# Kernel tuning notes

Measured on AMD Instinct MI355X. Metric: run time of the kernel, lower is better.

Reference implementation:

```python
import jax, jax.numpy as jnp
import numpy as np

D_MODEL = 1024
NUM_HEADS = 16
D_HEAD = D_MODEL // NUM_HEADS
D_FF = 4096
BATCH = 2
SEQ = 2048
EPS = 1e-5


def setup_inputs() -> dict:
    key = jax.random.key(0)
    ks = jax.random.split(key, 10)
    def tn(k, shape, std):
        # truncated normal in [-3*std, 3*std]
        return std * jax.random.truncated_normal(k, -3.0, 3.0, shape, dtype=jnp.float32)
    sd_attn = float(np.sqrt(2.0 / (D_MODEL + D_MODEL)))
    sd_ff1 = float(np.sqrt(2.0 / (D_MODEL + D_FF)))
    sd_ff2 = float(np.sqrt(2.0 / (D_FF + D_MODEL)))
    return {
        "x": jax.random.normal(ks[0], (BATCH, SEQ, D_MODEL), dtype=jnp.float32),
        "Wq": tn(ks[1], (D_MODEL, D_MODEL), sd_attn),
        "Wk": tn(ks[2], (D_MODEL, D_MODEL), sd_attn),
        "Wv": tn(ks[3], (D_MODEL, D_MODEL), sd_attn),
        "Wo": tn(ks[4], (D_MODEL, D_MODEL), sd_attn),
        "W1": tn(ks[5], (D_FF, D_MODEL), sd_ff1),
        "W2": tn(ks[6], (D_MODEL, D_FF), sd_ff2),
        "W3": tn(ks[7], (D_FF, D_MODEL), sd_ff1),
        "g1": tn(ks[8], (D_MODEL,), 1.0),
        "g2": tn(ks[9], (D_MODEL,), 1.0),
    }


def rmsnorm(x, g):
    xf = x.astype(jnp.float32)
    rms = jnp.sqrt(jnp.mean(xf * xf, axis=-1, keepdims=True) + EPS)
    return (xf / rms * g).astype(x.dtype)


def attention(x, Wq, Wk, Wv, Wo):
    B, S, D = x.shape
    def heads(t):  # [B,S,D] -> [B,H,S,dh]
        return t.reshape(B, S, NUM_HEADS, D_HEAD).transpose(0, 2, 1, 3)
    q = heads(jnp.einsum('oi,bsi->bso', Wq, x))
    k = heads(jnp.einsum('oi,bsi->bso', Wk, x))
    v = heads(jnp.einsum('oi,bsi->bso', Wv, x))
    logits = jnp.einsum('bhqd,bhkd->bhqk', q, k)
    mask = jnp.tril(jnp.ones((S, S), dtype=bool))
    logits = jnp.where(mask, logits, -jnp.inf)
    attn = jax.nn.softmax(logits / jnp.sqrt(jnp.float32(D_HEAD)), axis=-1)
    o = jnp.einsum('bhqk,bhkd->bhqd', attn, v)
    o = o.transpose(0, 2, 1, 3).reshape(B, S, D)
    return jnp.einsum('oi,bsi->bso', Wo, o)


def swiglu(x, W1, W2, W3):
    h1 = jnp.einsum('fi,bsi->bsf', W1, x)
    h3 = jnp.einsum('fi,bsi->bsf', W3, x)
    h = h1 * jax.nn.sigmoid(h1) * h3
    return jnp.einsum('of,bsf->bso', W2, h)


def reference(x, Wq, Wk, Wv, Wo, W1, W2, W3, g1, g2):
    x = x + attention(rmsnorm(x, g1), Wq, Wk, Wv, Wo)
    x = x + swiglu(rmsnorm(x, g2), W1, W2, W3)
    return x
```

## Files before the change

### kernel.cpp

```cpp
#include <hip/hip_runtime.h>
#include <hip/hip_bf16.h>

#define DM 1024
#define NH 16
#define DH 64
#define DFF 4096
#define NBATCH 2
#define SEQL 2048
#define MTOK (NBATCH*SEQL)

typedef float f32x4 __attribute__((ext_vector_type(4)));
typedef __bf16 bf16x8 __attribute__((ext_vector_type(8)));
typedef unsigned short u16;
typedef unsigned int u32;
typedef unsigned short u16x4 __attribute__((ext_vector_type(4)));
typedef unsigned short u16x8 __attribute__((ext_vector_type(8)));
typedef unsigned int u32x4 __attribute__((ext_vector_type(4)));

__device__ __forceinline__ u16 f2bf(float f) {
    u32 u = __builtin_bit_cast(u32, f);
    return (u16)((u + 0x7fffu + ((u >> 16) & 1u)) >> 16);
}
__device__ __forceinline__ float bf2f(u16 h) {
    return __builtin_bit_cast(float, (u32)h << 16);
}
__device__ __forceinline__ f32x4 mfma16(bf16x8 a, bf16x8 b, f32x4 c) {
    return __builtin_amdgcn_mfma_f32_16x16x32_bf16(a, b, c, 0, 0, 0);
}
__device__ __forceinline__ void gload16(const void* g, void* l) {
    __builtin_amdgcn_global_load_lds(
        (const __attribute__((address_space(1))) unsigned int*)g,
        (__attribute__((address_space(3))) unsigned int*)l, 16, 0, 0);
}

template<bool PRE>
__device__ __forceinline__ void gemm_core(
    const u16* __restrict__ Ah, const u16* __restrict__ Al,
    const u16* __restrict__ Bh, const u16* __restrict__ Bl,
    const float* __restrict__ W,
    int K, int m0, int n0,
    u16* lsAh, u16* lsAl, u16* lsBh, u16* lsBl,
    f32x4 acc[4][4])
{
    const int t = threadIdx.x;
    const int lane = t & 63;
    const int wv = t >> 6;
    const int wm = ((t >> 7) & 1) * 64;
    const int wn = ((t >> 6) & 1) * 64;
    const int lrow = lane & 15;
    const int lk = lane >> 4;
    const f32x4 FZ = {0.f, 0.f, 0.f, 0.f};
#pragma unroll
    for (int i = 0; i < 4; ++i)
#pragma unroll
        for (int j = 0; j < 4; ++j) acc[i][j] = FZ;

    for (int k0 = 0; k0 < K; k0 += 64) {
        if (PRE) {
#pragma unroll
            for (int p = 0; p < 4; ++p) {
                const int seg = wv * 4 + p;
                const int row = seg * 8 + (lane >> 3);
                const int g = (lane & 7) ^ (row & 7);
                const size_t sa = (size_t)(m0 + row) * K + k0 + g * 8;
                const size_t sb = (size_t)(n0 + row) * K + k0 + g * 8;
                gload16(Ah + sa, lsAh + seg * 512);
                gload16(Al + sa, lsAl + seg * 512);
                gload16(Bh + sb, lsBh + seg * 512);
                gload16(Bl + sb, lsBl + seg * 512);
            }
        } else {
#pragma unroll
            for (int j = 0; j < 4; ++j) {
                const int row = (t >> 3) + j * 32;
                const int chk = t & 7;
                const size_t src = (size_t)(m0 + row) * K + k0 + chk * 8;
                const int di = row * 64 + ((chk ^ (row & 7)) << 3);
                *reinterpret_cast<u16x8*>(&lsAh[di]) = *reinterpret_cast<const u16x8*>(&Ah[src]);
                *reinterpret_cast<u16x8*>(&lsAl[di]) = *reinterpret_cast<const u16x8*>(&Al[src]);
            }
#pragma unroll
            for (int j = 0; j < 8; ++j) {
                const int id = t + j * 256;
                const int row = id >> 4;
                const int f4 = id & 15;
                const f32x4 wv4 = *reinterpret_cast<const f32x4*>(&W[(size_t)(n0 + row) * K + k0 + f4 * 4]);
                u16x4 hh, ll;
#pragma unroll
                for (int e = 0; e < 4; ++e) {
                    const u16 hi = f2bf(wv4[e]);
                    hh[e] = hi;
                    ll[e] = f2bf(wv4[e] - bf2f(hi));
                }
                const int kc = f4 * 4;
                const int di = row * 64 + ((((kc >> 3) ^ (row & 7))) << 3) + (kc & 7);
                *reinterpret_cast<u16x4*>(&lsBh[di]) = hh;
                *reinterpret_cast<u16x4*>(&lsBl[di]) = ll;
            }
        }
        __syncthreads();
#pragma unroll
        for (int ks = 0; ks < 2; ++ks) {
            bf16x8 ah[4], al[4], bh[4], bl[4];
#pragma unroll
            for (int i = 0; i < 4; ++i) {
                const int ra = wm + i * 16 + lrow;
                const int ia = ra * 64 + ((((lk + ks * 4) ^ (ra & 7))) << 3);
                ah[i] = *reinterpret_cast<const bf16x8*>(&lsAh[ia]);
                al[i] = *reinterpret_cast<const bf16x8*>(&lsAl[ia]);
                const int rb = wn + i * 16 + lrow;
                const int ib = rb * 64 + ((((lk + ks * 4) ^ (rb & 7))) << 3);
                bh[i] = *reinterpret_cast<const bf16x8*>(&lsBh[ib]);
                bl[i] = *reinterpret_cast<const bf16x8*>(&lsBl[ib]);
            }
#pragma unroll
            for (int i = 0; i < 4; ++i)
#pragma unroll
                for (int j = 0; j < 4; ++j) {
                    acc[i][j] = mfma16(ah[i], bh[j], acc[i][j]);
                    acc[i][j] = mfma16(al[i], bh[j], acc[i][j]);
                    acc[i][j] = mfma16(ah[i], bl[j], acc[i][j]);
                }
        }
        __syncthreads();
    }
}

template <class F>
__device__ __forceinline__ void epilogue(const f32x4 acc[4][4], int m0, int n0, F f) {
    const int lane = threadIdx.x & 63;
    const int wm = ((threadIdx.x >> 7) & 1) * 64;
    const int wn = ((threadIdx.x >> 6) & 1) * 64;
#pragma unroll
    for (int i = 0; i < 4; ++i)
#pragma unroll
        for (int j = 0; j < 4; ++j)
#pragma unroll
            for (int r = 0; r < 4; ++r) {
                const int m = m0 + wm + i * 16 + ((lane >> 4) << 2) + r;
                const int o = n0 + wn + j * 16 + (lane & 15);
                f(m, o, acc[i][j][r]);
            }
}

__global__ __launch_bounds__(256) void k_splitw(
    const float* __restrict__ src, u16* __restrict__ dh, u16* __restrict__ dl, int n)
{
    const int i = (blockIdx.x * 256 + threadIdx.x) * 8;
    if (i + 8 > n) return;
    const f32x4 a = *reinterpret_cast<const f32x4*>(src + i);
    const f32x4 b = *reinterpret_cast<const f32x4*>(src + i + 4);
    u16x8 hh, ll;
#pragma unroll
    for (int e = 0; e < 4; ++e) {
        const u16 h0 = f2bf(a[e]);
        hh[e] = h0; ll[e] = f2bf(a[e] - bf2f(h0));
        const u16 h1 = f2bf(b[e]);
        hh[4 + e] = h1; ll[4 + e] = f2bf(b[e] - bf2f(h1));
    }
    *reinterpret_cast<u16x8*>(dh + i) = hh;
    *reinterpret_cast<u16x8*>(dl + i) = ll;
}

__global__ __launch_bounds__(256) void k_rmsnorm(
    const float* __restrict__ x, const float* __restrict__ g,
    u16* __restrict__ oh, u16* __restrict__ ol)
{
    const int row = blockIdx.x * 4 + (threadIdx.x >> 6);
    const int lane = threadIdx.x & 63;
    const float* xr = x + (size_t)row * DM;
    f32x4 v[4];
    float ss = 0.f;
#pragma unroll
    for (int j = 0; j < 4; ++j) {
        v[j] = *reinterpret_cast<const f32x4*>(&xr[(lane + j * 64) * 4]);
        ss += v[j][0] * v[j][0] + v[j][1] * v[j][1] + v[j][2] * v[j][2] + v[j][3] * v[j][3];
    }
#pragma unroll
    for (int off = 32; off > 0; off >>= 1) ss += __shfl_xor(ss, off, 64);
    const float sc = 1.0f / sqrtf(ss * (1.0f / (float)DM) + 1e-5f);
#pragma unroll
    for (int j = 0; j < 4; ++j) {
        const int c0 = (lane + j * 64) * 4;
        const f32x4 gv = *reinterpret_cast<const f32x4*>(&g[c0]);
        u16x4 hh, ll;
#pragma unroll
        for (int e = 0; e < 4; ++e) {
            const float y = v[j][e] * sc * gv[e];
            const u16 hi = f2bf(y);
            hh[e] = hi;
            ll[e] = f2bf(y - bf2f(hi));
        }
        *reinterpret_cast<u16x4*>(&oh[(size_t)row * DM + c0]) = hh;
        *reinterpret_cast<u16x4*>(&ol[(size_t)row * DM + c0]) = ll;
    }
}

template<bool PRE>
__global__ __launch_bounds__(256) void k_qkv(
    const u16* __restrict__ Ah, const u16* __restrict__ Al,
    const float* __restrict__ Wq, const float* __restrict__ Wk, const float* __restrict__ Wv,
    const u16* __restrict__ swqh, const u16* __restrict__ swql,
    const u16* __restrict__ swkh, const u16* __restrict__ swkl,
    const u16* __restrict__ swvh, const u16* __restrict__ swvl,
    u16* __restrict__ qh, u16* __restrict__ ql, u16* __restrict__ kh, u16* __restrict__ kl,
    u16* __restrict__ vth, u16* __restrict__ vtl)
{
    __shared__ __align__(16) u16 lsAh[128 * 64], lsAl[128 * 64], lsBh[128 * 64], lsBl[128 * 64];
    const int m0 = blockIdx.x * 128;
    const int ng = blockIdx.y * 128;
    const int proj = ng >> 10;
    const int n0 = ng & 1023;
    const float* W = (proj == 0) ? Wq : ((proj == 1) ? Wk : Wv);
    const u16* Bh = (proj == 0) ? swqh : ((proj == 1) ? swkh : swvh);
    const u16* Bl = (proj == 0) ? swql : ((proj == 1) ? swkl : swvl);
    f32x4 acc[4][4];
    gemm_core<PRE>(Ah, Al, Bh, Bl, W, DM, m0, n0, lsAh, lsAl, lsBh, lsBl, acc);
    if (proj < 2) {
        u16* oph = (proj == 0) ? qh : kh;
        u16* opl = (proj == 0) ? ql : kl;
        epilogue(acc, m0, n0, [&](int m, int o, float val) {
            const int b = m >> 11, s = m & (SEQL - 1);
            const int hd = o >> 6, d = o & 63;
            const size_t idx = (((size_t)b * NH + hd) * SEQL + s) * DH + d;
            const u16 hi = f2bf(val);
            oph[idx] = hi;
            opl[idx] = f2bf(val - bf2f(hi));
        });
    } else {
        epilogue(acc, m0, n0, [&](int m, int o, float val) {
            const int b = m >> 11, s = m & (SEQL - 1);
            const int hd = o >> 6, d = o & 63;
            const size_t idx = (((size_t)b * NH + hd) * DH + d) * SEQL + s;
            const u16 hi = f2bf(val);
            vth[idx] = hi;
            vtl[idx] = f2bf(val - bf2f(hi));
        });
    }
}

template<bool PRE>
__global__ __launch_bounds__(256) void k_oproj(
    const u16* __restrict__ Ah, const u16* __restrict__ Al,
    const float* __restrict__ Wo, const u16* __restrict__ Bh, const u16* __restrict__ Bl,
    const float* __restrict__ xres, float* __restrict__ out)
{
    __shared__ __align__(16) u16 lsAh[128 * 64], lsAl[128 * 64], lsBh[128 * 64], lsBl[128 * 64];
    const int m0 = blockIdx.x * 128;
    const int n0 = blockIdx.y * 128;
    f32x4 acc[4][4];
    gemm_core<PRE>(Ah, Al, Bh, Bl, Wo, DM, m0, n0, lsAh, lsAl, lsBh, lsBl, acc);
    epilogue(acc, m0, n0, [&](int m, int o, float val) {
        const size_t idx = (size_t)m * DM + o;
        out[idx] = xres[idx] + val;
    });
}

template<bool PRE>
__global__ __launch_bounds__(256) void k_ffn1(
    const u16* __restrict__ Ah, const u16* __restrict__ Al,
    const float* __restrict__ W1, const u16* __restrict__ Bh, const u16* __restrict__ Bl,
    u16* __restrict__ hh, u16* __restrict__ hl)
{
    __shared__ __align__(16) u16 lsAh[128 * 64], lsAl[128 * 64], lsBh[128 * 64], lsBl[128 * 64];
    const int m0 = blockIdx.x * 128;
    const int n0 = blockIdx.y * 128;
    f32x4 acc[4][4];
    gemm_core<PRE>(Ah, Al, Bh, Bl, W1, DM, m0, n0, lsAh, lsAl, lsBh, lsBl, acc);
    epilogue(acc, m0, n0, [&](int m, int o, float val) {
        const size_t idx = (size_t)m * DFF + o;
        const u16 hi = f2bf(val);
        hh[idx] = hi;
        hl[idx] = f2bf(val - bf2f(hi));
    });
}

template<bool PRE>
__global__ __launch_bounds__(256) void k_ffn3(
    const u16* __restrict__ Ah, const u16* __restrict__ Al,
    const float* __restrict__ W3, const u16* __restrict__ Bh, const u16* __restrict__ Bl,
    u16* __restrict__ hh, u16* __restrict__ hl)
{
    __shared__ __align__(16) u16 lsAh[128 * 64], lsAl[128 * 64], lsBh[128 * 64], lsBl[128 * 64];
    const int m0 = blockIdx.x * 128;
    const int n0 = blockIdx.y * 128;
    f32x4 acc[4][4];
    gemm_core<PRE>(Ah, Al, Bh, Bl, W3, DM, m0, n0, lsAh, lsAl, lsBh, lsBl, acc);
    epilogue(acc, m0, n0, [&](int m, int o, float val) {
        const size_t idx = (size_t)m * DFF + o;
        const float h1 = bf2f(hh[idx]) + bf2f(hl[idx]);
        const float sg = 1.0f / (1.0f + expf(-h1));
        const float hv = h1 * sg * val;
        const u16 hi = f2bf(hv);
        hh[idx] = hi;
        hl[idx] = f2bf(hv - bf2f(hi));
    });
}

template<bool PRE>
__global__ __launch_bounds__(256) void k_ffn2(
    const u16* __restrict__ Ah, const u16* __restrict__ Al,
    const float* __restrict__ W2, const u16* __restrict__ Bh, const u16* __restrict__ Bl,
    float* __restrict__ out)
{
    __shared__ __align__(16) u16 lsAh[128 * 64], lsAl[128 * 64], lsBh[128 * 64], lsBl[128 * 64];
    const int m0 = blockIdx.x * 128;
    const int n0 = blockIdx.y * 128;
    f32x4 acc[4][4];
    gemm_core<PRE>(Ah, Al, Bh, Bl, W2, DFF, m0, n0, lsAh, lsAl, lsBh, lsBl, acc);
    epilogue(acc, m0, n0, [&](int m, int o, float val) {
        const size_t idx = (size_t)m * DM + o;
        out[idx] = out[idx] + val;
    });
}

__global__ __launch_bounds__(256) void k_attn(
    const u16* __restrict__ gqh, const u16* __restrict__ gql,
    const u16* __restrict__ gkh, const u16* __restrict__ gkl,
    const u16* __restrict__ gvth, const u16* __restrict__ gvtl,
    u16* __restrict__ aoh, u16* __restrict__ aol)
{
    __shared__ __align__(16) u16 sKh[2][4096], sKl[2][4096], sVh[2][4096], sVl[2][4096];
    __shared__ __align__(16) u32 Pw[4][16 * 64];
    const int t = threadIdx.x, lane = t & 63, wid = t >> 6;
    const int lrow = lane & 15, lk = lane >> 4;
    const int bh = blockIdx.y;
    const int pr = blockIdx.x;
    const size_t base = (size_t)bh * SEQL * DH;
    const f32x4 FZ = {0.f, 0.f, 0.f, 0.f};
    const int b = bh >> 4, hd = bh & 15;

    auto stage = [&](int buf, int kvt) {
        const int kv0 = kvt << 6;
#pragma unroll
        for (int p = 0; p < 2; ++p) {
            const int seg = wid * 2 + p;
            const int row = seg * 8 + (lane >> 3);
            const int g = (lane & 7) ^ (row & 7);
            const size_t sk = base + (size_t)(kv0 + row) * DH + g * 8;
            const size_t sv = base + (size_t)row * SEQL + kv0 + g * 8;
            gload16(gkh + sk, &sKh[buf][seg * 512]);
            gload16(gkl + sk, &sKl[buf][seg * 512]);
            gload16(gvth + sv, &sVh[buf][seg * 512]);
            gload16(gvtl + sv, &sVl[buf][seg * 512]);
        }
    };

    for (int hf = 0; hf < 2; ++hf) {
        const int qt = hf ? (31 - pr) : pr;
        const int qw = qt * 64 + wid * 16;
        bf16x8 Qh[2], Ql[2];
#pragma unroll
        for (int ks = 0; ks < 2; ++ks) {
            const size_t off = base + (size_t)(qw + lrow) * DH + ks * 32 + lk * 8;
            Qh[ks] = *reinterpret_cast<const bf16x8*>(&gqh[off]);
            Ql[ks] = *reinterpret_cast<const bf16x8*>(&gql[off]);
        }
        float mr[4], lr[4];
        f32x4 Oa[4];
#pragma unroll
        for (int r = 0; r < 4; ++r) { mr[r] = -1.0e30f; lr[r] = 0.f; }
#pragma unroll
        for (int n = 0; n < 4; ++n) Oa[n] = FZ;

        const int ntile = qt + 1;
        stage(0, 0);
        __syncthreads();
        int buf = 0;
        for (int kvt = 0; kvt < ntile; ++kvt) {
            if (kvt + 1 < ntile) stage(buf ^ 1, kvt + 1);
            const int kv0 = kvt << 6;
            f32x4 S[4];
#pragma unroll
            for (int nf = 0; nf < 4; ++nf) S[nf] = FZ;
#pragma unroll
            for (int ks = 0; ks < 2; ++ks) {
                bf16x8 kbh[4], kbl[4];
#pragma unroll
                for (int nf = 0; nf < 4; ++nf) {
                    const int row = nf * 16 + lrow;
                    const int idx = row * 64 + (((lk + ks * 4) ^ (row & 7)) << 3);
                    kbh[nf] = *reinterpret_cast<const bf16x8*>(&sKh[buf][idx]);
                    kbl[nf] = *reinterpret_cast<const bf16x8*>(&sKl[buf][idx]);
                }
#pragma unroll
                for (int nf = 0; nf < 4; ++nf) {
                    S[nf] = mfma16(Qh[ks], kbh[nf], S[nf]);
                    S[nf] = mfma16(Ql[ks], kbh[nf], S[nf]);
                    S[nf] = mfma16(Qh[ks], kbl[nf], S[nf]);
                }
            }
#pragma unroll
            for (int r = 0; r < 4; ++r) {
                const int qrow = qw + (lk << 2) + r;
                float rmx = -3.0e38f;
#pragma unroll
                for (int nf = 0; nf < 4; ++nf) {
                    const int col = kv0 + nf * 16 + lrow;
                    const float tv = (col <= qrow) ? S[nf][r] * 0.125f : -3.0e38f;
                    S[nf][r] = tv;
                    rmx = fmaxf(rmx, tv);
                }
#pragma unroll
                for (int off = 8; off > 0; off >>= 1) rmx = fmaxf(rmx, __shfl_xor(rmx, off, 16));
                const float mnew = fmaxf(mr[r], rmx);
                const float alpha = exp2f((mr[r] - mnew) * 1.44269504f);
                mr[r] = mnew;
                float rsum = 0.f;
#pragma unroll
                for (int nf = 0; nf < 4; ++nf) {
                    const float p = exp2f((S[nf][r] - mnew) * 1.44269504f);
                    S[nf][r] = p;
                    rsum += p;
                }
#pragma unroll
                for (int off = 8; off > 0; off >>= 1) rsum += __shfl_xor(rsum, off, 16);
                lr[r] = lr[r] * alpha + rsum;
#pragma unroll
                for (int n = 0; n < 4; ++n) Oa[n][r] *= alpha;
                const int prow = (lk << 2) + r;
#pragma unroll
                for (int nf = 0; nf < 4; ++nf) {
                    const float p = S[nf][r];
                    const u16 phi = f2bf(p);
                    const u16 plo = f2bf(p - bf2f(phi));
                    const int pcol = nf * 16 + lrow;
                    Pw[wid][prow * 64 + ((((pcol >> 3) ^ (prow & 7))) << 3) + (pcol & 7)] =
                        (u32)phi | ((u32)plo << 16);
                }
            }
            asm volatile("s_waitcnt lgkmcnt(0)" ::: "memory");
#pragma unroll
            for (int ks = 0; ks < 2; ++ks) {
                const int row = lrow;
                const int c = (lk + ks * 4) ^ (row & 7);
                const u32* pp = &Pw[wid][row * 64 + (c << 3)];
                const u32x4 w0 = *reinterpret_cast<const u32x4*>(pp);
                const u32x4 w1 = *reinterpret_cast<const u32x4*>(pp + 4);
                union { u16 s[8]; bf16x8 v; } uh, ul;
#pragma unroll
                for (int e = 0; e < 4; ++e) {
                    uh.s[e] = (u16)(w0[e] & 0xffffu); ul.s[e] = (u16)(w0[e] >> 16);
                    uh.s[e + 4] = (u16)(w1[e] & 0xffffu); ul.s[e + 4] = (u16)(w1[e] >> 16);
                }
                bf16x8 vbh[4], vbl[4];
#pragma unroll
                for (int n = 0; n < 4; ++n) {
                    const int vr = n * 16 + lrow;
                    const int idx = vr * 64 + (((lk + ks * 4) ^ (vr & 7)) << 3);
                    vbh[n] = *reinterpret_cast<const bf16x8*>(&sVh[buf][idx]);
                    vbl[n] = *reinterpret_cast<const bf16x8*>(&sVl[buf][idx]);
                }
#pragma unroll
                for (int n = 0; n < 4; ++n) {
                    Oa[n] = mfma16(uh.v, vbh[n], Oa[n]);
                    Oa[n] = mfma16(ul.v, vbh[n], Oa[n]);
                    Oa[n] = mfma16(uh.v, vbl[n], Oa[n]);
                }
            }
            __syncthreads();
            buf ^= 1;
        }
#pragma unroll
        for (int r = 0; r < 4; ++r) {
            const float inv = 1.0f / lr[r];
            const int s = qw + (lk << 2) + r;
#pragma unroll
            for (int n = 0; n < 4; ++n) {
                const float o = Oa[n][r] * inv;
                const int d = hd * 64 + n * 16 + lrow;
                const size_t idx = ((size_t)b * SEQL + s) * DM + d;
                const u16 hi = f2bf(o);
                aoh[idx] = hi;
                aol[idx] = f2bf(o - bf2f(hi));
            }
        }
    }
}

extern "C" void kernel_launch(void* const* d_in, const int* in_sizes, int n_in,
                              void* d_out, int out_size, void* d_ws, size_t ws_size,
                              hipStream_t stream) {
    (void)in_sizes; (void)n_in; (void)out_size;
    const float* x  = (const float*)d_in[0];
    const float* Wq = (const float*)d_in[1];
    const float* Wk = (const float*)d_in[2];
    const float* Wv = (const float*)d_in[3];
    const float* Wo = (const float*)d_in[4];
    const float* W1 = (const float*)d_in[5];
    const float* W2 = (const float*)d_in[6];
    const float* W3 = (const float*)d_in[7];
    const float* g1 = (const float*)d_in[8];
    const float* g2 = (const float*)d_in[9];
    float* out = (float*)d_out;
    char* w = (char*)d_ws;
    const size_t MB = 1024ull * 1024ull;
    u16* xnh = (u16*)(w + 0 * MB);
    u16* xnl = (u16*)(w + 8 * MB);
    u16* qh  = (u16*)(w + 16 * MB);
    u16* ql  = (u16*)(w + 24 * MB);
    u16* kh  = (u16*)(w + 32 * MB);
    u16* kl  = (u16*)(w + 40 * MB);
    u16* vth = (u16*)(w + 48 * MB);
    u16* vtl = (u16*)(w + 56 * MB);
    u16* aoh = (u16*)(w + 64 * MB);
    u16* aol = (u16*)(w + 72 * MB);
    u16* hh  = (u16*)(w + 16 * MB);
    u16* hl  = (u16*)(w + 48 * MB);
    const bool pre = ws_size >= (144ull << 20);
    u16* wsp = (u16*)(w + 80 * MB);
    u16* wqh = wsp;                  u16* wql = wqh + (1u << 20);
    u16* wkh = wql + (1u << 20);     u16* wkl = wkh + (1u << 20);
    u16* wvh = wkl + (1u << 20);     u16* wvl = wvh + (1u << 20);
    u16* woh = wvl + (1u << 20);     u16* wol = woh + (1u << 20);
    u16* w1h = wol + (1u << 20);     u16* w1l = w1h + (4u << 20);
    u16* w2h = w1l + (4u << 20);     u16* w2l = w2h + (4u << 20);
    u16* w3h = w2l + (4u << 20);     u16* w3l = w3h + (4u << 20);

    if (pre) {
        k_splitw<<<512, 256, 0, stream>>>(Wq, wqh, wql, 1 << 20);
        k_splitw<<<512, 256, 0, stream>>>(Wk, wkh, wkl, 1 << 20);
        k_splitw<<<512, 256, 0, stream>>>(Wv, wvh, wvl, 1 << 20);
        k_splitw<<<512, 256, 0, stream>>>(Wo, woh, wol, 1 << 20);
        k_splitw<<<2048, 256, 0, stream>>>(W1, w1h, w1l, 4 << 20);
        k_splitw<<<2048, 256, 0, stream>>>(W2, w2h, w2l, 4 << 20);
        k_splitw<<<2048, 256, 0, stream>>>(W3, w3h, w3l, 4 << 20);
    }
    k_rmsnorm<<<dim3(MTOK / 4), 256, 0, stream>>>(x, g1, xnh, xnl);
    if (pre) {
        k_qkv<true><<<dim3(32, 24), 256, 0, stream>>>(xnh, xnl, Wq, Wk, Wv,
            wqh, wql, wkh, wkl, wvh, wvl, qh, ql, kh, kl, vth, vtl);
        k_attn<<<dim3(16, 32), 256, 0, stream>>>(qh, ql, kh, kl, vth, vtl, aoh, aol);
        k_oproj<true><<<dim3(32, 8), 256, 0, stream>>>(aoh, aol, Wo, woh, wol, x, out);
        k_rmsnorm<<<dim3(MTOK / 4), 256, 0, stream>>>(out, g2, xnh, xnl);
        k_ffn1<true><<<dim3(32, 32), 256, 0, stream>>>(xnh, xnl, W1, w1h, w1l, hh, hl);
        k_ffn3<true><<<dim3(32, 32), 256, 0, stream>>>(xnh, xnl, W3, w3h, w3l, hh, hl);
        k_ffn2<true><<<dim3(32, 8), 256, 0, stream>>>(hh, hl, W2, w2h, w2l, out);
    } else {
        k_qkv<false><<<dim3(32, 24), 256, 0, stream>>>(xnh, xnl, Wq, Wk, Wv,
            nullptr, nullptr, nullptr, nullptr, nullptr, nullptr, qh, ql, kh, kl, vth, vtl);
        k_attn<<<dim3(16, 32), 256, 0, stream>>>(qh, ql, kh, kl, vth, vtl, aoh, aol);
        k_oproj<false><<<dim3(32, 8), 256, 0, stream>>>(aoh, aol, Wo, nullptr, nullptr, x, out);
        k_rmsnorm<<<dim3(MTOK / 4), 256, 0, stream>>>(out, g2, xnh, xnl);
        k_ffn1<false><<<dim3(32, 32), 256, 0, stream>>>(xnh, xnl, W1, nullptr, nullptr, hh, hl);
        k_ffn3<false><<<dim3(32, 32), 256, 0, stream>>>(xnh, xnl, W3, nullptr, nullptr, hh, hl);
        k_ffn2<false><<<dim3(32, 8), 256, 0, stream>>>(hh, hl, W2, nullptr, nullptr, out);
    }
}
```

Before: 715.5 us.

## Double-buffer GEMM LDS with K=32 tiles and fuse FFN1/FFN3 into one kernel

```diff
diff --git a/kernel.cpp b/kernel.cpp
--- a/kernel.cpp
+++ b/kernel.cpp
@@ -33,11 +33,9 @@
         (__attribute__((address_space(3))) unsigned int*)l, 16, 0, 0);
 }
 
-template<bool PRE>
 __device__ __forceinline__ void gemm_core(
     const u16* __restrict__ Ah, const u16* __restrict__ Al,
     const u16* __restrict__ Bh, const u16* __restrict__ Bl,
-    const float* __restrict__ W,
     int K, int m0, int n0,
     u16* lsAh, u16* lsAl, u16* lsBh, u16* lsBl,
     f32x4 acc[4][4])
@@ -55,76 +53,57 @@
 #pragma unroll
         for (int j = 0; j < 4; ++j) acc[i][j] = FZ;
 
-    for (int k0 = 0; k0 < K; k0 += 64) {
-        if (PRE) {
-#pragma unroll
-            for (int p = 0; p < 4; ++p) {
-                const int seg = wv * 4 + p;
-                const int row = seg * 8 + (lane >> 3);
-                const int g = (lane & 7) ^ (row & 7);
-                const size_t sa = (size_t)(m0 + row) * K + k0 + g * 8;
-                const size_t sb = (size_t)(n0 + row) * K + k0 + g * 8;
-                gload16(Ah + sa, lsAh + seg * 512);
-                gload16(Al + sa, lsAl + seg * 512);
-                gload16(Bh + sb, lsBh + seg * 512);
-                gload16(Bl + sb, lsBl + seg * 512);
-            }
-        } else {
+    const int NT = K >> 5;
+    const int sc = (lane & 3) * 8;
+    const int rsub = lane >> 2;
+
+    auto stage = [&](int buf, int kt) {
+        const int k0 = kt << 5;
+#pragma unroll
+        for (int p = 0; p < 2; ++p) {
+            const int seg = wv * 2 + p;
+            const int row = seg * 16 + rsub;
+            const size_t sa = (size_t)(m0 + row) * K + k0 + sc;
+            const size_t sb = (size_t)(n0 + row) * K + k0 + sc;
+            const int d = buf * 4096 + seg * 512;
+            gload16(Ah + sa, lsAh + d);
+            gload16(Al + sa, lsAl + d);
+            gload16(Bh + sb, lsBh + d);
+            gload16(Bl + sb, lsBl + d);
+        }
+    };
+
+    stage(0, 0);
+    __syncthreads();
+    int buf = 0;
+    for (int kt = 0; kt < NT; ++kt) {
+        if (kt + 1 < NT) stage(buf ^ 1, kt + 1);
+        bf16x8 ah[4], al[4], bh[4], bl[4];
+#pragma unroll
+        for (int i = 0; i < 4; ++i) {
+            const int ia = buf * 4096 + (wm + i * 16 + lrow) * 32 + lk * 8;
+            ah[i] = *reinterpret_cast<const bf16x8*>(&lsAh[ia]);
+            al[i] = *reinterpret_cast<const bf16x8*>(&lsAl[ia]);
+            const int ib = buf * 4096 + (wn + i * 16 + lrow) * 32 + lk * 8;
+            bh[i] = *reinterpret_cast<const bf16x8*>(&lsBh[ib]);
+            bl[i] = *reinterpret_cast<const bf16x8*>(&lsBl[ib]);
+        }
+#pragma unroll
+        for (int i = 0; i < 4; ++i)
 #pragma unroll
             for (int j = 0; j < 4; ++j) {
-                const int row = (t >> 3) + j * 32;
-                const int chk = t & 7;
-                const size_t src = (size_t)(m0 + row) * K + k0 + chk * 8;
-                const int di = row * 64 + ((chk ^ (row & 7)) << 3);
-                *reinterpret_cast<u16x8*>(&lsAh[di]) = *reinterpret_cast<const u16x8*>(&Ah[src]);
-                *reinterpret_cast<u16x8*>(&lsAl[di]) = *reinterpret_cast<const u16x8*>(&Al[src]);
-            }
-#pragma unroll
-            for (int j = 0; j < 8; ++j) {
-                const int id = t + j * 256;
-                const int row = id >> 4;
-                const int f4 = id & 15;
-                const f32x4 wv4 = *reinterpret_cast<const f32x4*>(&W[(size_t)(n0 + row) * K + k0 + f4 * 4]);
-                u16x4 hh, ll;
-#pragma unroll
-                for (int e = 0; e < 4; ++e) {
-                    const u16 hi = f2bf(wv4[e]);
-                    hh[e] = hi;
-                    ll[e] = f2bf(wv4[e] - bf2f(hi));
-                }
-                const int kc = f4 * 4;
-                const int di = row * 64 + ((((kc >> 3) ^ (row & 7))) << 3) + (kc & 7);
-                *reinterpret_cast<u16x4*>(&lsBh[di]) = hh;
-                *reinterpret_cast<u16x4*>(&lsBl[di]) = ll;
-            }
-        }
+                acc[i][j] = mfma16(ah[i], bh[j], acc[i][j]);
+                acc[i][j] = mfma16(al[i], bh[j], acc[i][j]);
+                acc[i][j] = mfma16(ah[i], bl[j], acc[i][j]);
+            }
         __syncthreads();
-#pragma unroll
-        for (int ks = 0; ks < 2; ++ks) {
-            bf16x8 ah[4], al[4], bh[4], bl[4];
-#pragma unroll
-            for (int i = 0; i < 4; ++i) {
-                const int ra = wm + i * 16 + lrow;
-                const int ia = ra * 64 + ((((lk + ks * 4) ^ (ra & 7))) << 3);
-                ah[i] = *reinterpret_cast<const bf16x8*>(&lsAh[ia]);
-                al[i] = *reinterpret_cast<const bf16x8*>(&lsAl[ia]);
-                const int rb = wn + i * 16 + lrow;
-                const int ib = rb * 64 + ((((lk + ks * 4) ^ (rb & 7))) << 3);
-                bh[i] = *reinterpret_cast<const bf16x8*>(&lsBh[ib]);
-                bl[i] = *reinterpret_cast<const bf16x8*>(&lsBl[ib]);
-            }
-#pragma unroll
-            for (int i = 0; i < 4; ++i)
-#pragma unroll
-                for (int j = 0; j < 4; ++j) {
-                    acc[i][j] = mfma16(ah[i], bh[j], acc[i][j]);
-                    acc[i][j] = mfma16(al[i], bh[j], acc[i][j]);
-                    acc[i][j] = mfma16(ah[i], bl[j], acc[i][j]);
-                }
-        }
-        __syncthreads();
+        buf ^= 1;
     }
 }
+
+#define GEMM_LDS \
+    __shared__ __align__(16) u16 lsAh[2 * 4096], lsAl[2 * 4096], \
+                                 lsBh[2 * 4096], lsBl[2 * 4096];
 
 template <class F>
 __device__ __forceinline__ void epilogue(const f32x4 acc[4][4], int m0, int n0, F f) {
@@ -196,26 +175,23 @@
     }
 }
 
-template<bool PRE>
 __global__ __launch_bounds__(256) void k_qkv(
     const u16* __restrict__ Ah, const u16* __restrict__ Al,
-    const float* __restrict__ Wq, const float* __restrict__ Wk, const float* __restrict__ Wv,
     const u16* __restrict__ swqh, const u16* __restrict__ swql,
     const u16* __restrict__ swkh, const u16* __restrict__ swkl,
     const u16* __restrict__ swvh, const u16* __restrict__ swvl,
     u16* __restrict__ qh, u16* __restrict__ ql, u16* __restrict__ kh, u16* __restrict__ kl,
     u16* __restrict__ vth, u16* __restrict__ vtl)
 {
-    __shared__ __align__(16) u16 lsAh[128 * 64], lsAl[128 * 64], lsBh[128 * 64], lsBl[128 * 64];
+    GEMM_LDS
     const int m0 = blockIdx.x * 128;
     const int ng = blockIdx.y * 128;
     const int proj = ng >> 10;
     const int n0 = ng & 1023;
-    const float* W = (proj == 0) ? Wq : ((proj == 1) ? Wk : Wv);
     const u16* Bh = (proj == 0) ? swqh : ((proj == 1) ? swkh : swvh);
     const u16* Bl = (proj == 0) ? swql : ((proj == 1) ? swkl : swvl);
     f32x4 acc[4][4];
-    gemm_core<PRE>(Ah, Al, Bh, Bl, W, DM, m0, n0, lsAh, lsAl, lsBh, lsBl, acc);
+    gemm_core(Ah, Al, Bh, Bl, DM, m0, n0, lsAh, lsAl, lsBh, lsBl, acc);
     if (proj < 2) {
         u16* oph = (proj == 0) ? qh : kh;
         u16* opl = (proj == 0) ? ql : kl;
@@ -239,75 +215,66 @@
     }
 }
 
-template<bool PRE>
 __global__ __launch_bounds__(256) void k_oproj(
     const u16* __restrict__ Ah, const u16* __restrict__ Al,
-    const float* __restrict__ Wo, const u16* __restrict__ Bh, const u16* __restrict__ Bl,
+    const u16* __restrict__ Bh, const u16* __restrict__ Bl,
     const float* __restrict__ xres, float* __restrict__ out)
 {
-    __shared__ __align__(16) u16 lsAh[128 * 64], lsAl[128 * 64], lsBh[128 * 64], lsBl[128 * 64];
+    GEMM_LDS
     const int m0 = blockIdx.x * 128;
     const int n0 = blockIdx.y * 128;
     f32x4 acc[4][4];
-    gemm_core<PRE>(Ah, Al, Bh, Bl, Wo, DM, m0, n0, lsAh, lsAl, lsBh, lsBl, acc);
+    gemm_core(Ah, Al, Bh, Bl, DM, m0, n0, lsAh, lsAl, lsBh, lsBl, acc);
     epilogue(acc, m0, n0, [&](int m, int o, float val) {
         const size_t idx = (size_t)m * DM + o;
         out[idx] = xres[idx] + val;
     });
 }
 
-template<bool PRE>
-__global__ __launch_bounds__(256) void k_ffn1(
+__global__ __launch_bounds__(256, 2) void k_ffn13(
     const u16* __restrict__ Ah, const u16* __restrict__ Al,
-    const float* __restrict__ W1, const u16* __restrict__ Bh, const u16* __restrict__ Bl,
+    const u16* __restrict__ B1h, const u16* __restrict__ B1l,
+    const u16* __restrict__ B3h, const u16* __restrict__ B3l,
     u16* __restrict__ hh, u16* __restrict__ hl)
 {
-    __shared__ __align__(16) u16 lsAh[128 * 64], lsAl[128 * 64], lsBh[128 * 64], lsBl[128 * 64];
+    GEMM_LDS
+    const int m0 = blockIdx.x * 128;
+    const int n0 = blockIdx.y * 128;
+    f32x4 acc1[4][4], acc3[4][4];
+    gemm_core(Ah, Al, B1h, B1l, DM, m0, n0, lsAh, lsAl, lsBh, lsBl, acc1);
+    gemm_core(Ah, Al, B3h, B3l, DM, m0, n0, lsAh, lsAl, lsBh, lsBl, acc3);
+    const int lane = threadIdx.x & 63;
+    const int wm = ((threadIdx.x >> 7) & 1) * 64;
+    const int wn = ((threadIdx.x >> 6) & 1) * 64;
+#pragma unroll
+    for (int i = 0; i < 4; ++i)
+#pragma unroll
+        for (int j = 0; j < 4; ++j)
+#pragma unroll
+            for (int r = 0; r < 4; ++r) {
+                const int m = m0 + wm + i * 16 + ((lane >> 4) << 2) + r;
+                const int o = n0 + wn + j * 16 + (lane & 15);
+                const float h1 = acc1[i][j][r];
+                const float h3 = acc3[i][j][r];
+                const float sg = 1.0f / (1.0f + expf(-h1));
+                const float hv = h1 * sg * h3;
+                const size_t idx = (size_t)m * DFF + o;
+                const u16 hi = f2bf(hv);
+                hh[idx] = hi;
+                hl[idx] = f2bf(hv - bf2f(hi));
+            }
+}
+
+__global__ __launch_bounds__(256) void k_ffn2(
+    const u16* __restrict__ Ah, const u16* __restrict__ Al,
+    const u16* __restrict__ Bh, const u16* __restrict__ Bl,
+    float* __restrict__ out)
+{
+    GEMM_LDS
     const int m0 = blockIdx.x * 128;
     const int n0 = blockIdx.y * 128;
     f32x4 acc[4][4];
-    gemm_core<PRE>(Ah, Al, Bh, Bl, W1, DM, m0, n0, lsAh, lsAl, lsBh, lsBl, acc);
-    epilogue(acc, m0, n0, [&](int m, int o, float val) {
-        const size_t idx = (size_t)m * DFF + o;
-        const u16 hi = f2bf(val);
-        hh[idx] = hi;
-        hl[idx] = f2bf(val - bf2f(hi));
-    });
-}
-
-template<bool PRE>
-__global__ __launch_bounds__(256) void k_ffn3(
-    const u16* __restrict__ Ah, const u16* __restrict__ Al,
-    const float* __restrict__ W3, const u16* __restrict__ Bh, const u16* __restrict__ Bl,
-    u16* __restrict__ hh, u16* __restrict__ hl)
-{
-    __shared__ __align__(16) u16 lsAh[128 * 64], lsAl[128 * 64], lsBh[128 * 64], lsBl[128 * 64];
-    const int m0 = blockIdx.x * 128;
-    const int n0 = blockIdx.y * 128;
-    f32x4 acc[4][4];
-    gemm_core<PRE>(Ah, Al, Bh, Bl, W3, DM, m0, n0, lsAh, lsAl, lsBh, lsBl, acc);
-    epilogue(acc, m0, n0, [&](int m, int o, float val) {
-        const size_t idx = (size_t)m * DFF + o;
-        const float h1 = bf2f(hh[idx]) + bf2f(hl[idx]);
-        const float sg = 1.0f / (1.0f + expf(-h1));
-        const float hv = h1 * sg * val;
-        const u16 hi = f2bf(hv);
-        hh[idx] = hi;
-        hl[idx] = f2bf(hv - bf2f(hi));
-    });
-}
-
-template<bool PRE>
-__global__ __launch_bounds__(256) void k_ffn2(
-    const u16* __restrict__ Ah, const u16* __restrict__ Al,
-    const float* __restrict__ W2, const u16* __restrict__ Bh, const u16* __restrict__ Bl,
-    float* __restrict__ out)
-{
-    __shared__ __align__(16) u16 lsAh[128 * 64], lsAl[128 * 64], lsBh[128 * 64], lsBl[128 * 64];
-    const int m0 = blockIdx.x * 128;
-    const int n0 = blockIdx.y * 128;
-    f32x4 acc[4][4];
-    gemm_core<PRE>(Ah, Al, Bh, Bl, W2, DFF, m0, n0, lsAh, lsAl, lsBh, lsBl, acc);
+    gemm_core(Ah, Al, Bh, Bl, DFF, m0, n0, lsAh, lsAl, lsBh, lsBl, acc);
     epilogue(acc, m0, n0, [&](int m, int o, float val) {
         const size_t idx = (size_t)m * DM + o;
         out[idx] = out[idx] + val;
@@ -481,7 +448,7 @@
 extern "C" void kernel_launch(void* const* d_in, const int* in_sizes, int n_in,
                               void* d_out, int out_size, void* d_ws, size_t ws_size,
                               hipStream_t stream) {
-    (void)in_sizes; (void)n_in; (void)out_size;
+    (void)in_sizes; (void)n_in; (void)out_size; (void)ws_size;
     const float* x  = (const float*)d_in[0];
     const float* Wq = (const float*)d_in[1];
     const float* Wk = (const float*)d_in[2];
@@ -507,7 +474,6 @@
     u16* aol = (u16*)(w + 72 * MB);
     u16* hh  = (u16*)(w + 16 * MB);
     u16* hl  = (u16*)(w + 48 * MB);
-    const bool pre = ws_size >= (144ull << 20);
     u16* wsp = (u16*)(w + 80 * MB);
     u16* wqh = wsp;                  u16* wql = wqh + (1u << 20);
     u16* wkh = wql + (1u << 20);     u16* wkl = wkh + (1u << 20);
@@ -517,33 +483,20 @@
     u16* w2h = w1l + (4u << 20);     u16* w2l = w2h + (4u << 20);
     u16* w3h = w2l + (4u << 20);     u16* w3l = w3h + (4u << 20);
 
-    if (pre) {
-        k_splitw<<<512, 256, 0, stream>>>(Wq, wqh, wql, 1 << 20);
-        k_splitw<<<512, 256, 0, stream>>>(Wk, wkh, wkl, 1 << 20);
-        k_splitw<<<512, 256, 0, stream>>>(Wv, wvh, wvl, 1 << 20);
-        k_splitw<<<512, 256, 0, stream>>>(Wo, woh, wol, 1 << 20);
-        k_splitw<<<2048, 256, 0, stream>>>(W1, w1h, w1l, 4 << 20);
-        k_splitw<<<2048, 256, 0, stream>>>(W2, w2h, w2l, 4 << 20);
-        k_splitw<<<2048, 256, 0, stream>>>(W3, w3h, w3l, 4 << 20);
-    }
+    k_splitw<<<512, 256, 0, stream>>>(Wq, wqh, wql, 1 << 20);
+    k_splitw<<<512, 256, 0, stream>>>(Wk, wkh, wkl, 1 << 20);
+    k_splitw<<<512, 256, 0, stream>>>(Wv, wvh, wvl, 1 << 20);
+    k_splitw<<<512, 256, 0, stream>>>(Wo, woh, wol, 1 << 20);
+    k_splitw<<<2048, 256, 0, stream>>>(W1, w1h, w1l, 4 << 20);
+    k_splitw<<<2048, 256, 0, stream>>>(W2, w2h, w2l, 4 << 20);
+    k_splitw<<<2048, 256, 0, stream>>>(W3, w3h, w3l, 4 << 20);
+
     k_rmsnorm<<<dim3(MTOK / 4), 256, 0, stream>>>(x, g1, xnh, xnl);
-    if (pre) {
-        k_qkv<true><<<dim3(32, 24), 256, 0, stream>>>(xnh, xnl, Wq, Wk, Wv,
-            wqh, wql, wkh, wkl, wvh, wvl, qh, ql, kh, kl, vth, vtl);
-        k_attn<<<dim3(16, 32), 256, 0, stream>>>(qh, ql, kh, kl, vth, vtl, aoh, aol);
-        k_oproj<true><<<dim3(32, 8), 256, 0, stream>>>(aoh, aol, Wo, woh, wol, x, out);
-        k_rmsnorm<<<dim3(MTOK / 4), 256, 0, stream>>>(out, g2, xnh, xnl);
-        k_ffn1<true><<<dim3(32, 32), 256, 0, stream>>>(xnh, xnl, W1, w1h, w1l, hh, hl);
-        k_ffn3<true><<<dim3(32, 32), 256, 0, stream>>>(xnh, xnl, W3, w3h, w3l, hh, hl);
-        k_ffn2<true><<<dim3(32, 8), 256, 0, stream>>>(hh, hl, W2, w2h, w2l, out);
-    } else {
-        k_qkv<false><<<dim3(32, 24), 256, 0, stream>>>(xnh, xnl, Wq, Wk, Wv,
-            nullptr, nullptr, nullptr, nullptr, nullptr, nullptr, qh, ql, kh, kl, vth, vtl);
-        k_attn<<<dim3(16, 32), 256, 0, stream>>>(qh, ql, kh, kl, vth, vtl, aoh, aol);
-        k_oproj<false><<<dim3(32, 8), 256, 0, stream>>>(aoh, aol, Wo, nullptr, nullptr, x, out);
-        k_rmsnorm<<<dim3(MTOK / 4), 256, 0, stream>>>(out, g2, xnh, xnl);
-        k_ffn1<false><<<dim3(32, 32), 256, 0, stream>>>(xnh, xnl, W1, nullptr, nullptr, hh, hl);
-        k_ffn3<false><<<dim3(32, 32), 256, 0, stream>>>(xnh, xnl, W3, nullptr, nullptr, hh, hl);
-        k_ffn2<false><<<dim3(32, 8), 256, 0, stream>>>(hh, hl, W2, nullptr, nullptr, out);
-    }
-}
+    k_qkv<<<dim3(32, 24), 256, 0, stream>>>(xnh, xnl,
+        wqh, wql, wkh, wkl, wvh, wvl, qh, ql, kh, kl, vth, vtl);
+    k_attn<<<dim3(16, 32), 256, 0, stream>>>(qh, ql, kh, kl, vth, vtl, aoh, aol);
+    k_oproj<<<dim3(32, 8), 256, 0, stream>>>(aoh, aol, woh, wol, x, out);
+    k_rmsnorm<<<dim3(MTOK / 4), 256, 0, stream>>>(out, g2, xnh, xnl);
+    k_ffn13<<<dim3(32, 32), 256, 0, stream>>>(xnh, xnl, w1h, w1l, w3h, w3l, hh, hl);
+    k_ffn2<<<dim3(32, 8), 256, 0, stream>>>(hh, hl, w2h, w2l, out);
+}
```

Result: slower. 835.8 us (+16.8%).
